# Kernel optimization log

Hardware: AMD Instinct MI355X
Metric: run time of the kernel (lower is better)

## Reference

```python
import jax, jax.numpy as jnp
import numpy as np

EMBED_DIM = 1024
VOCAB = 32000
B, S = 4, 4096


def setup_inputs() -> dict:
    key = jax.random.key(0)
    ks = jax.random.split(key, 6)
    scale = 1.0 / np.sqrt(EMBED_DIM)
    x = jax.random.randint(ks[0], (B, S), 0, VOCAB, dtype=jnp.int64)
    embed = jax.random.normal(ks[1], (VOCAB, EMBED_DIM), dtype=jnp.float32)
    qkv_w = jax.random.normal(ks[2], (EMBED_DIM, 3 * EMBED_DIM), dtype=jnp.float32) * scale
    qkv_b = jnp.zeros((3 * EMBED_DIM,), dtype=jnp.float32)
    out_w = jax.random.normal(ks[3], (EMBED_DIM, VOCAB), dtype=jnp.float32) * scale
    out_b = jnp.zeros((VOCAB,), dtype=jnp.float32)
    return {"x": x, "embed": embed, "qkv_w": qkv_w, "qkv_b": qkv_b,
            "out_w": out_w, "out_b": out_b}


def reference(x, embed, qkv_w, qkv_b, out_w, out_b):
    h = embed[x]                                   # [B,S,D] token embedding lookup
    qkv = h @ qkv_w + qkv_b                        # [B,S,3D]
    qkv = qkv.reshape(B, S, 3, EMBED_DIM)
    q, k, v = qkv[:, :, 0], qkv[:, :, 1], qkv[:, :, 2]
    logits = jnp.einsum('bqd,bkd->bqk', q, k) / jnp.sqrt(jnp.float32(EMBED_DIM))
    attn = jax.nn.softmax(logits, axis=-1)         # [B,S,S] full score matrix (as in source)
    out = jnp.einsum('bqk,bkd->bqd', attn, v)
    h = out + h                                    # residual
    # source applies output projection then slices last token; equivalent to
    # projecting the last-token hidden only.
    return h[:, -1, :] @ out_w + out_b             # [B, vocab]
```

## Files before the change

kernel.cpp:

```cpp
#include <hip/hip_runtime.h>
#include <hip/hip_bf16.h>

typedef __bf16 bf16;
typedef __bf16 bf16x4 __attribute__((ext_vector_type(4)));
typedef __bf16 bf16x8 __attribute__((ext_vector_type(8)));
typedef float floatx4 __attribute__((ext_vector_type(4)));

#define EMBED 1024
#define VOCAB 32000
#define BB    4
#define SS    4096
#define NTOK  (BB * SS)
#define NKV   2048
#define NSEG  16

__device__ __forceinline__ void async_copy16(void* lds, const void* g) {
    __builtin_amdgcn_global_load_lds(
        (const __attribute__((address_space(1))) unsigned int*)g,
        (__attribute__((address_space(3))) unsigned int*)lds, 16, 0, 0);
}

__global__ void gather_embed(const int* __restrict__ x,
                             const float* __restrict__ embed,
                             bf16* __restrict__ h,
                             float* __restrict__ h_last,
                             float* __restrict__ h_final) {
    int t = blockIdx.x;
    int tid = threadIdx.x;
    int row = x[t];
    const float4* src = (const float4*)(embed + (size_t)row * EMBED);
    float4 v = src[tid];
    bf16x4 o; o.x = (bf16)v.x; o.y = (bf16)v.y; o.z = (bf16)v.z; o.w = (bf16)v.w;
    *(bf16x4*)(h + (size_t)t * EMBED + tid * 4) = o;
    if ((t & (SS - 1)) == SS - 1) {
        int b = t >> 12;
        *(float4*)(h_last  + b * EMBED + tid * 4) = v;
        *(float4*)(h_final + b * EMBED + tid * 4) = v;
    }
}

__global__ void wkvt_transpose(const float* __restrict__ qkv_w,
                               bf16* __restrict__ WkvT) {
    __shared__ float T[32][33];
    int n0 = blockIdx.x * 32, d0 = blockIdx.y * 32;
    int tid = threadIdx.x;
    int c = tid & 31, r = tid >> 5;
#pragma unroll
    for (int i = 0; i < 4; ++i) {
        int d = r + i * 8;
        T[c][d] = qkv_w[(size_t)(d0 + d) * (3 * EMBED) + EMBED + n0 + c];
    }
    __syncthreads();
#pragma unroll
    for (int i = 0; i < 4; ++i) {
        int n = r + i * 8;
        WkvT[(size_t)(n0 + n) * EMBED + d0 + c] = (bf16)T[n][c];
    }
}

__global__ void q_gemm(const float* __restrict__ h_last,
                       const float* __restrict__ qkv_w,
                       float* __restrict__ qpart) {
    __shared__ float hs[BB * 64];
    int tid = threadIdx.x;
    int seg = blockIdx.x, d0 = seg * 64;
    hs[tid] = h_last[(tid >> 6) * EMBED + d0 + (tid & 63)];
    __syncthreads();
    int j0 = tid * 4;
    floatx4 acc[BB];
#pragma unroll
    for (int b = 0; b < BB; ++b) acc[b] = (floatx4)0.0f;
#pragma unroll 4
    for (int dd = 0; dd < 64; ++dd) {
        float4 w = *(const float4*)(qkv_w + (size_t)(d0 + dd) * (3 * EMBED) + j0);
#pragma unroll
        for (int b = 0; b < BB; ++b) {
            float hv = hs[b * 64 + dd];
            acc[b][0] += hv * w.x; acc[b][1] += hv * w.y;
            acc[b][2] += hv * w.z; acc[b][3] += hv * w.w;
        }
    }
#pragma unroll
    for (int b = 0; b < BB; ++b)
        *(floatx4*)(qpart + ((size_t)seg * BB + b) * EMBED + j0) = acc[b];
}

__global__ void q_reduce(const float* __restrict__ qpart,
                         const float* __restrict__ qkv_b,
                         float* __restrict__ q) {
    int k = blockIdx.x * 256 + threadIdx.x;
    int b = k >> 10, d = k & (EMBED - 1);
    float s = qkv_b[d];
#pragma unroll
    for (int sg = 0; sg < NSEG; ++sg) s += qpart[((size_t)sg * BB + b) * EMBED + d];
    q[k] = s;
}

__global__ __launch_bounds__(512, 1) void gemm_kv(
    const bf16* __restrict__ A,
    const bf16* __restrict__ BT,
    const float* __restrict__ bias,
    bf16* __restrict__ C) {
    __shared__ __align__(16) bf16 SA[2][2][256 * 32];
    __shared__ __align__(16) bf16 SB[2][2][256 * 32];

    const int tid  = threadIdx.x;
    const int wave = tid >> 6, lane = tid & 63;
    const int wm = wave >> 2, wn = wave & 3;
    const int l16 = lane & 15, quad = lane >> 4;
    const int swz_l = (l16 & 3) ^ ((l16 >> 2) & 3);
    const int a_base = (wm * 128 + l16) * 32 + (quad ^ swz_l) * 8;
    const int b_base = (wn * 64  + l16) * 32 + (quad ^ swz_l) * 8;

    const bf16* Abase = A  + (size_t)blockIdx.x * 256 * EMBED;
    const bf16* Bbase = BT + (size_t)blockIdx.y * 256 * EMBED;

    floatx4 acc[8][4];
#pragma unroll
    for (int m = 0; m < 8; ++m)
#pragma unroll
        for (int n = 0; n < 4; ++n) acc[m][n] = (floatx4)0.0f;

    bf16x8 af[4], af2[4], bfr[4];

#define STG(KH, KT) do { \
    int c_ = wave * 128 + lane; \
    int r_ = c_ >> 2, sw_ = (r_ & 3) ^ ((r_ >> 2) & 3); \
    size_t go_ = (size_t)r_ * EMBED + (KT) * 64 + (KH) * 32 + ((c_ & 3) ^ sw_) * 8; \
    async_copy16(&SA[KH][(KT) & 1][c_ * 8], Abase + go_); \
    async_copy16(&SB[KH][(KT) & 1][c_ * 8], Bbase + go_); \
    c_ += 64; r_ = c_ >> 2; sw_ = (r_ & 3) ^ ((r_ >> 2) & 3); \
    go_ = (size_t)r_ * EMBED + (KT) * 64 + (KH) * 32 + ((c_ & 3) ^ sw_) * 8; \
    async_copy16(&SA[KH][(KT) & 1][c_ * 8], Abase + go_); \
    async_copy16(&SB[KH][(KT) & 1][c_ * 8], Bbase + go_); \
} while (0)

#define NOSTG() do { } while (0)

#define HSTEP(KH, PAR, STG_BODY, WN) do { \
    __builtin_amdgcn_sched_barrier(0); \
    asm volatile("s_waitcnt vmcnt(" #WN ")" ::: "memory"); \
    __builtin_amdgcn_s_barrier(); \
    __builtin_amdgcn_sched_barrier(0); \
    STG_BODY; \
    { const bf16* pa_ = &SA[KH][PAR][a_base]; \
      const bf16* pb_ = &SB[KH][PAR][b_base]; \
      _Pragma("unroll") \
      for (int i_ = 0; i_ < 4; ++i_) af [i_] = *(const bf16x8*)(pa_ + i_ * 512); \
      _Pragma("unroll") \
      for (int i_ = 0; i_ < 4; ++i_) bfr[i_] = *(const bf16x8*)(pb_ + i_ * 512); \
      _Pragma("unroll") \
      for (int i_ = 0; i_ < 4; ++i_) af2[i_] = *(const bf16x8*)(pa_ + 2048 + i_ * 512); } \
    __builtin_amdgcn_s_setprio(1); \
    _Pragma("unroll") \
    for (int mf_ = 0; mf_ < 4; ++mf_) \
    _Pragma("unroll") \
    for (int nf_ = 0; nf_ < 4; ++nf_) \
        acc[mf_][nf_] = __builtin_amdgcn_mfma_f32_16x16x32_bf16( \
            af[mf_], bfr[nf_], acc[mf_][nf_], 0, 0, 0); \
    _Pragma("unroll") \
    for (int mf_ = 0; mf_ < 4; ++mf_) \
    _Pragma("unroll") \
    for (int nf_ = 0; nf_ < 4; ++nf_) \
        acc[4 + mf_][nf_] = __builtin_amdgcn_mfma_f32_16x16x32_bf16( \
            af2[mf_], bfr[nf_], acc[4 + mf_][nf_], 0, 0, 0); \
    __builtin_amdgcn_s_setprio(0); \
} while (0)

    STG(0, 0); STG(1, 0); STG(0, 1);

#pragma unroll 1
    for (int kk = 0; kk < 7; ++kk) {
        const int t1 = 2 * kk + 1;
        HSTEP(0, 0, STG(1, t1),     8);
        HSTEP(1, 0, STG(0, t1 + 1), 8);
        HSTEP(0, 1, STG(1, t1 + 1), 8);
        HSTEP(1, 1, STG(0, t1 + 2), 8);
    }
    HSTEP(0, 0, STG(1, 15), 8);
    HSTEP(1, 0, NOSTG(),    8);
    HSTEP(0, 1, NOSTG(),    4);
    HSTEP(1, 1, NOSTG(),    0);

    const int crow0 = blockIdx.x * 256 + wm * 128;
    const int ccol0 = blockIdx.y * 256 + wn * 64;
    float bsv[4];
#pragma unroll
    for (int nf = 0; nf < 4; ++nf) bsv[nf] = bias[ccol0 + nf * 16 + l16];
#pragma unroll
    for (int fm = 0; fm < 8; ++fm)
#pragma unroll
        for (int nf = 0; nf < 4; ++nf) {
            int col = ccol0 + nf * 16 + l16;
#pragma unroll
            for (int r = 0; r < 4; ++r) {
                int row = crow0 + fm * 16 + quad * 4 + r;
                C[(size_t)row * NKV + col] = (bf16)(acc[fm][nf][r] + bsv[nf]);
            }
        }
#undef STG
#undef NOSTG
#undef HSTEP
}

__global__ void attn_logits(const bf16* __restrict__ KV,
                            const float* __restrict__ q,
                            float* __restrict__ logits) {
    __shared__ float qs[EMBED];
    int b = blockIdx.x >> 10;
    int t = (blockIdx.x & 1023) * 4 + (threadIdx.x >> 6);
    int lane = threadIdx.x & 63;
    *(float4*)(qs + threadIdx.x * 4) = *(const float4*)(q + b * EMBED + threadIdx.x * 4);
    __syncthreads();
    const bf16* Krow = KV + (size_t)(b * SS + t) * NKV;
    float sum = 0.0f;
#pragma unroll
    for (int i = 0; i < 2; ++i) {
        int d0 = i * 512 + lane * 8;
        bf16x8 kv8 = *(const bf16x8*)(Krow + d0);
        float4 qa = *(const float4*)(qs + d0);
        float4 qc = *(const float4*)(qs + d0 + 4);
        sum += qa.x * (float)kv8[0] + qa.y * (float)kv8[1] +
               qa.z * (float)kv8[2] + qa.w * (float)kv8[3] +
               qc.x * (float)kv8[4] + qc.y * (float)kv8[5] +
               qc.z * (float)kv8[6] + qc.w * (float)kv8[7];
    }
#pragma unroll
    for (int o = 32; o; o >>= 1) sum += __shfl_down(sum, o);
    if (lane == 0) logits[b * SS + t] = sum * 0.03125f;
}

__global__ void softmax_k(const float* __restrict__ logits,
                          float* __restrict__ wts) {
    int b = blockIdx.x, tid = threadIdx.x;
    __shared__ float redm[16], reds[16];
    const float* l = logits + b * SS;
    float x0 = l[tid], x1 = l[tid + 1024], x2 = l[tid + 2048], x3 = l[tid + 3072];
    float m = fmaxf(fmaxf(x0, x1), fmaxf(x2, x3));
#pragma unroll
    for (int o = 32; o; o >>= 1) m = fmaxf(m, __shfl_down(m, o));
    if ((tid & 63) == 0) redm[tid >> 6] = m;
    __syncthreads();
    float M = redm[0];
#pragma unroll
    for (int i = 1; i < 16; ++i) M = fmaxf(M, redm[i]);
    float e0 = expf(x0 - M), e1 = expf(x1 - M), e2 = expf(x2 - M), e3 = expf(x3 - M);
    float s = e0 + e1 + e2 + e3;
#pragma unroll
    for (int o = 32; o; o >>= 1) s += __shfl_down(s, o);
    if ((tid & 63) == 0) reds[tid >> 6] = s;
    __syncthreads();
    float S = 0.0f;
#pragma unroll
    for (int i = 0; i < 16; ++i) S += reds[i];
    float inv = 1.0f / S;
    float* w = wts + b * SS;
    w[tid] = e0 * inv; w[tid + 1024] = e1 * inv;
    w[tid + 2048] = e2 * inv; w[tid + 3072] = e3 * inv;
}

__global__ void attn_av(const bf16* __restrict__ KV,
                        const float* __restrict__ wts,
                        float* __restrict__ avpart) {
    int b = blockIdx.x >> 6, ts = blockIdx.x & 63;
    int tid = threadIdx.x;
    __shared__ float wsh[64];
    if (tid < 64) wsh[tid] = wts[b * SS + ts * 64 + tid];
    __syncthreads();
    int d = tid * 4;
    const bf16* Vb = KV + (size_t)(b * SS + ts * 64) * NKV + EMBED + d;
    float a0 = 0, a1 = 0, a2 = 0, a3 = 0;
#pragma unroll 4
    for (int j = 0; j < 64; ++j) {
        bf16x4 v = *(const bf16x4*)(Vb + (size_t)j * NKV);
        float w = wsh[j];
        a0 += w * (float)v.x; a1 += w * (float)v.y;
        a2 += w * (float)v.z; a3 += w * (float)v.w;
    }
    float4 o; o.x = a0; o.y = a1; o.z = a2; o.w = a3;
    *(float4*)(avpart + (size_t)(b * 64 + ts) * EMBED + d) = o;
}

__global__ void av_reduce(const float* __restrict__ avpart,
                          float* __restrict__ h_final) {
    int i = blockIdx.x * 256 + threadIdx.x;
    int b = i >> 10, d = i & (EMBED - 1);
    float s = 0.0f;
#pragma unroll
    for (int ts = 0; ts < 64; ++ts)
        s += avpart[(size_t)(b * 64 + ts) * EMBED + d];
    h_final[i] += s;
}

__global__ void out_gemm(const float* __restrict__ h_final,
                         const float* __restrict__ out_w,
                         float* __restrict__ opart) {
    __shared__ float hs[BB * 64];
    int tid = threadIdx.x;
    int seg = blockIdx.y, d0 = seg * 64;
    hs[tid] = h_final[(tid >> 6) * EMBED + d0 + (tid & 63)];
    __syncthreads();
    int j0 = blockIdx.x * 1024 + tid * 4;
    if (j0 >= VOCAB) return;
    floatx4 acc[BB];
#pragma unroll
    for (int b = 0; b < BB; ++b) acc[b] = (floatx4)0.0f;
#pragma unroll 4
    for (int dd = 0; dd < 64; ++dd) {
        float4 w = *(const float4*)(out_w + (size_t)(d0 + dd) * VOCAB + j0);
#pragma unroll
        for (int b = 0; b < BB; ++b) {
            float hv = hs[b * 64 + dd];
            acc[b][0] += hv * w.x; acc[b][1] += hv * w.y;
            acc[b][2] += hv * w.z; acc[b][3] += hv * w.w;
        }
    }
#pragma unroll
    for (int b = 0; b < BB; ++b)
        *(floatx4*)(opart + ((size_t)seg * BB + b) * VOCAB + j0) = acc[b];
}

__global__ void out_reduce(const float* __restrict__ opart,
                           const float* __restrict__ out_b,
                           float* __restrict__ out) {
    int i = blockIdx.x * 256 + threadIdx.x;
    if (i >= BB * VOCAB) return;
    int b = i / VOCAB, j = i - b * VOCAB;
    float s = out_b[j];
#pragma unroll
    for (int sg = 0; sg < NSEG; ++sg) s += opart[((size_t)sg * BB + b) * VOCAB + j];
    out[i] = s;
}

extern "C" void kernel_launch(void* const* d_in, const int* in_sizes, int n_in,
                              void* d_out, int out_size, void* d_ws, size_t ws_size,
                              hipStream_t stream) {
    const int*   x      = (const int*)d_in[0];
    const float* embed  = (const float*)d_in[1];
    const float* qkv_w  = (const float*)d_in[2];
    const float* qkv_b  = (const float*)d_in[3];
    const float* out_w  = (const float*)d_in[4];
    const float* out_b  = (const float*)d_in[5];
    float* out = (float*)d_out;

    char* ws = (char*)d_ws;
    bf16*  h       = (bf16*)(ws);
    float* avpart  = (float*)(ws);
    float* opart   = (float*)(ws);
    bf16*  KV      = (bf16*)(ws + 33554432);
    bf16*  WkvT    = (bf16*)(ws + 100663296);
    float* h_last  = (float*)(ws + 104857600);
    float* h_final = (float*)(ws + 104873984);
    float* q       = (float*)(ws + 104890368);
    float* logits  = (float*)(ws + 104906752);
    float* wts     = (float*)(ws + 104972288);
    float* qpart   = (float*)(ws + 105037824);

    gather_embed<<<NTOK, 256, 0, stream>>>(x, embed, h, h_last, h_final);
    wkvt_transpose<<<dim3(64, 32), 256, 0, stream>>>(qkv_w, WkvT);
    q_gemm<<<NSEG, 256, 0, stream>>>(h_last, qkv_w, qpart);
    q_reduce<<<16, 256, 0, stream>>>(qpart, qkv_b, q);
    gemm_kv<<<dim3(NTOK / 256, NKV / 256), 512, 0, stream>>>(
        h, WkvT, qkv_b + EMBED, KV);
    attn_logits<<<SS, 256, 0, stream>>>(KV, q, logits);
    softmax_k<<<BB, 1024, 0, stream>>>(logits, wts);
    attn_av<<<256, 256, 0, stream>>>(KV, wts, avpart);
    av_reduce<<<16, 256, 0, stream>>>(avpart, h_final);
    out_gemm<<<dim3(32, NSEG), 256, 0, stream>>>(h_final, out_w, opart);
    out_reduce<<<(BB * VOCAB + 255) / 256, 256, 0, stream>>>(opart, out_b, out);
}
```

Measured before the change: 404.2 us.

## Deepen KV GEMM pipeline to four LDS stages with register double-buffered fragments

Reworks the K/V projection GEMM main loop so LDS holds four 32-wide K slices in flight instead of two double-buffered halves. Operand fragments for the next slice are read into a second register set while MFMAs run on the current set, so LDS reads overlap matrix math. The cost is more VGPRs for the duplicated fragments and an extra lgkmcnt wait per step. Register pressure could cause spills, and the synchronization has to stay correct.

```diff
diff --git a/kernel.cpp b/kernel.cpp
--- a/kernel.cpp
+++ b/kernel.cpp
@@ -101,8 +101,8 @@
     const bf16* __restrict__ BT,
     const float* __restrict__ bias,
     bf16* __restrict__ C) {
-    __shared__ __align__(16) bf16 SA[2][2][256 * 32];
-    __shared__ __align__(16) bf16 SB[2][2][256 * 32];
+    __shared__ __align__(16) bf16 SA[4][8192];
+    __shared__ __align__(16) bf16 SB[4][8192];
 
     const int tid  = threadIdx.x;
     const int wave = tid >> 6, lane = tid & 63;
@@ -121,66 +121,89 @@
 #pragma unroll
         for (int n = 0; n < 4; ++n) acc[m][n] = (floatx4)0.0f;
 
-    bf16x8 af[4], af2[4], bfr[4];
-
-#define STG(KH, KT) do { \
+    bf16x8 af0[4], af20[4], bf0[4];
+    bf16x8 af1[4], af21[4], bf1[4];
+
+#define STG(H) do { \
     int c_ = wave * 128 + lane; \
     int r_ = c_ >> 2, sw_ = (r_ & 3) ^ ((r_ >> 2) & 3); \
-    size_t go_ = (size_t)r_ * EMBED + (KT) * 64 + (KH) * 32 + ((c_ & 3) ^ sw_) * 8; \
-    async_copy16(&SA[KH][(KT) & 1][c_ * 8], Abase + go_); \
-    async_copy16(&SB[KH][(KT) & 1][c_ * 8], Bbase + go_); \
+    size_t go_ = (size_t)r_ * EMBED + (H) * 32 + ((c_ & 3) ^ sw_) * 8; \
+    async_copy16(&SA[(H) & 3][c_ * 8], Abase + go_); \
+    async_copy16(&SB[(H) & 3][c_ * 8], Bbase + go_); \
     c_ += 64; r_ = c_ >> 2; sw_ = (r_ & 3) ^ ((r_ >> 2) & 3); \
-    go_ = (size_t)r_ * EMBED + (KT) * 64 + (KH) * 32 + ((c_ & 3) ^ sw_) * 8; \
-    async_copy16(&SA[KH][(KT) & 1][c_ * 8], Abase + go_); \
-    async_copy16(&SB[KH][(KT) & 1][c_ * 8], Bbase + go_); \
+    go_ = (size_t)r_ * EMBED + (H) * 32 + ((c_ & 3) ^ sw_) * 8; \
+    async_copy16(&SA[(H) & 3][c_ * 8], Abase + go_); \
+    async_copy16(&SB[(H) & 3][c_ * 8], Bbase + go_); \
 } while (0)
 
-#define NOSTG() do { } while (0)
-
-#define HSTEP(KH, PAR, STG_BODY, WN) do { \
+#define RDF(H, AF, AF2, BF) do { \
+    const bf16* pa_ = &SA[(H) & 3][0] + a_base; \
+    const bf16* pb_ = &SB[(H) & 3][0] + b_base; \
+    _Pragma("unroll") \
+    for (int i_ = 0; i_ < 4; ++i_) AF[i_]  = *(const bf16x8*)(pa_ + i_ * 512); \
+    _Pragma("unroll") \
+    for (int i_ = 0; i_ < 4; ++i_) BF[i_]  = *(const bf16x8*)(pb_ + i_ * 512); \
+    _Pragma("unroll") \
+    for (int i_ = 0; i_ < 4; ++i_) AF2[i_] = *(const bf16x8*)(pa_ + 2048 + i_ * 512); \
+} while (0)
+
+#define MFMAH(AF, AF2, BF) do { \
+    __builtin_amdgcn_s_setprio(1); \
+    _Pragma("unroll") \
+    for (int mf_ = 0; mf_ < 4; ++mf_) \
+    _Pragma("unroll") \
+    for (int nf_ = 0; nf_ < 4; ++nf_) \
+        acc[mf_][nf_] = __builtin_amdgcn_mfma_f32_16x16x32_bf16( \
+            AF[mf_], BF[nf_], acc[mf_][nf_], 0, 0, 0); \
+    _Pragma("unroll") \
+    for (int mf_ = 0; mf_ < 4; ++mf_) \
+    _Pragma("unroll") \
+    for (int nf_ = 0; nf_ < 4; ++nf_) \
+        acc[4 + mf_][nf_] = __builtin_amdgcn_mfma_f32_16x16x32_bf16( \
+            AF2[mf_], BF[nf_], acc[4 + mf_][nf_], 0, 0, 0); \
+    __builtin_amdgcn_s_setprio(0); \
+} while (0)
+
+#define SYNC(VM) do { \
     __builtin_amdgcn_sched_barrier(0); \
-    asm volatile("s_waitcnt vmcnt(" #WN ")" ::: "memory"); \
+    asm volatile("s_waitcnt lgkmcnt(0)" ::: "memory"); \
+    asm volatile("s_waitcnt vmcnt(" #VM ")" ::: "memory"); \
     __builtin_amdgcn_s_barrier(); \
     __builtin_amdgcn_sched_barrier(0); \
-    STG_BODY; \
-    { const bf16* pa_ = &SA[KH][PAR][a_base]; \
-      const bf16* pb_ = &SB[KH][PAR][b_base]; \
-      _Pragma("unroll") \
-      for (int i_ = 0; i_ < 4; ++i_) af [i_] = *(const bf16x8*)(pa_ + i_ * 512); \
-      _Pragma("unroll") \
-      for (int i_ = 0; i_ < 4; ++i_) bfr[i_] = *(const bf16x8*)(pb_ + i_ * 512); \
-      _Pragma("unroll") \
-      for (int i_ = 0; i_ < 4; ++i_) af2[i_] = *(const bf16x8*)(pa_ + 2048 + i_ * 512); } \
-    __builtin_amdgcn_s_setprio(1); \
-    _Pragma("unroll") \
-    for (int mf_ = 0; mf_ < 4; ++mf_) \
-    _Pragma("unroll") \
-    for (int nf_ = 0; nf_ < 4; ++nf_) \
-        acc[mf_][nf_] = __builtin_amdgcn_mfma_f32_16x16x32_bf16( \
-            af[mf_], bfr[nf_], acc[mf_][nf_], 0, 0, 0); \
-    _Pragma("unroll") \
-    for (int mf_ = 0; mf_ < 4; ++mf_) \
-    _Pragma("unroll") \
-    for (int nf_ = 0; nf_ < 4; ++nf_) \
-        acc[4 + mf_][nf_] = __builtin_amdgcn_mfma_f32_16x16x32_bf16( \
-            af2[mf_], bfr[nf_], acc[4 + mf_][nf_], 0, 0, 0); \
-    __builtin_amdgcn_s_setprio(0); \
 } while (0)
 
-    STG(0, 0); STG(1, 0); STG(0, 1);
+    STG(0); STG(1); STG(2); STG(3);
+    __builtin_amdgcn_sched_barrier(0);
+    asm volatile("s_waitcnt vmcnt(8)" ::: "memory");
+    __builtin_amdgcn_s_barrier();
+    __builtin_amdgcn_sched_barrier(0);
+    RDF(0, af0, af20, bf0);
+    __builtin_amdgcn_sched_barrier(0);
+    asm volatile("s_waitcnt lgkmcnt(0)" ::: "memory");
+    __builtin_amdgcn_s_barrier();
+    __builtin_amdgcn_sched_barrier(0);
 
 #pragma unroll 1
-    for (int kk = 0; kk < 7; ++kk) {
-        const int t1 = 2 * kk + 1;
-        HSTEP(0, 0, STG(1, t1),     8);
-        HSTEP(1, 0, STG(0, t1 + 1), 8);
-        HSTEP(0, 1, STG(1, t1 + 1), 8);
-        HSTEP(1, 1, STG(0, t1 + 2), 8);
-    }
-    HSTEP(0, 0, STG(1, 15), 8);
-    HSTEP(1, 0, NOSTG(),    8);
-    HSTEP(0, 1, NOSTG(),    4);
-    HSTEP(1, 1, NOSTG(),    0);
+    for (int kk = 0; kk < 14; ++kk) {
+        const int H = 2 * kk;
+        STG(H + 4);
+        RDF(H + 1, af1, af21, bf1);
+        MFMAH(af0, af20, bf0);
+        SYNC(8);
+        STG(H + 5);
+        RDF(H + 2, af0, af20, bf0);
+        MFMAH(af1, af21, bf1);
+        SYNC(8);
+    }
+    RDF(29, af1, af21, bf1);
+    MFMAH(af0, af20, bf0);
+    SYNC(4);
+    RDF(30, af0, af20, bf0);
+    MFMAH(af1, af21, bf1);
+    SYNC(0);
+    RDF(31, af1, af21, bf1);
+    MFMAH(af0, af20, bf0);
+    MFMAH(af1, af21, bf1);
 
     const int crow0 = blockIdx.x * 256 + wm * 128;
     const int ccol0 = blockIdx.y * 256 + wn * 64;
@@ -199,8 +222,9 @@
             }
         }
 #undef STG
-#undef NOSTG
-#undef HSTEP
+#undef RDF
+#undef MFMAH
+#undef SYNC
 }
 
 __global__ void attn_logits(const bf16* __restrict__ KV,
```

After: 415.4 us. 2.8% more time.

## Fuse prep kernels, atomically accumulate AV output, single-pass output projection

Applied to the files above, without the earlier changes.

Merges the embedding gather, K/V weight transpose and Q projection into one launch, with the Q path reading last-token embeddings straight from the table. The attention-value kernel now atomically adds its partial sums into the residual buffer instead of writing partials for a separate reduce. The output projection is rewritten so each block covers 64 vocab columns over the full embedding, reducing within the block and adding the bias, which removes the partial buffer and the reduce kernel. This cuts four launches and the partial-buffer traffic, but the atomics make the summation order nondeterministic and the new GEMM loads out_w with scalar rather than vector reads.

```diff
diff --git a/kernel.cpp b/kernel.cpp
--- a/kernel.cpp
+++ b/kernel.cpp
@@ -20,69 +20,66 @@
         (__attribute__((address_space(3))) unsigned int*)lds, 16, 0, 0);
 }
 
-__global__ void gather_embed(const int* __restrict__ x,
-                             const float* __restrict__ embed,
-                             bf16* __restrict__ h,
-                             float* __restrict__ h_last,
-                             float* __restrict__ h_final) {
-    int t = blockIdx.x;
-    int tid = threadIdx.x;
-    int row = x[t];
-    const float4* src = (const float4*)(embed + (size_t)row * EMBED);
-    float4 v = src[tid];
-    bf16x4 o; o.x = (bf16)v.x; o.y = (bf16)v.y; o.z = (bf16)v.z; o.w = (bf16)v.w;
-    *(bf16x4*)(h + (size_t)t * EMBED + tid * 4) = o;
-    if ((t & (SS - 1)) == SS - 1) {
-        int b = t >> 12;
-        *(float4*)(h_last  + b * EMBED + tid * 4) = v;
-        *(float4*)(h_final + b * EMBED + tid * 4) = v;
-    }
-}
-
-__global__ void wkvt_transpose(const float* __restrict__ qkv_w,
-                               bf16* __restrict__ WkvT) {
+__global__ void prep(const int* __restrict__ x,
+                     const float* __restrict__ embed,
+                     const float* __restrict__ qkv_w,
+                     bf16* __restrict__ h,
+                     float* __restrict__ h_final,
+                     bf16* __restrict__ WkvT,
+                     float* __restrict__ qpart) {
     __shared__ float T[32][33];
-    int n0 = blockIdx.x * 32, d0 = blockIdx.y * 32;
-    int tid = threadIdx.x;
-    int c = tid & 31, r = tid >> 5;
-#pragma unroll
-    for (int i = 0; i < 4; ++i) {
-        int d = r + i * 8;
-        T[c][d] = qkv_w[(size_t)(d0 + d) * (3 * EMBED) + EMBED + n0 + c];
-    }
-    __syncthreads();
-#pragma unroll
-    for (int i = 0; i < 4; ++i) {
-        int n = r + i * 8;
-        WkvT[(size_t)(n0 + n) * EMBED + d0 + c] = (bf16)T[n][c];
-    }
-}
-
-__global__ void q_gemm(const float* __restrict__ h_last,
-                       const float* __restrict__ qkv_w,
-                       float* __restrict__ qpart) {
     __shared__ float hs[BB * 64];
-    int tid = threadIdx.x;
-    int seg = blockIdx.x, d0 = seg * 64;
-    hs[tid] = h_last[(tid >> 6) * EMBED + d0 + (tid & 63)];
-    __syncthreads();
-    int j0 = tid * 4;
-    floatx4 acc[BB];
-#pragma unroll
-    for (int b = 0; b < BB; ++b) acc[b] = (floatx4)0.0f;
+    const int blk = blockIdx.x, tid = threadIdx.x;
+
+    if (blk < NTOK) {
+        int row = x[blk];
+        const float4* src = (const float4*)(embed + (size_t)row * EMBED);
+        float4 v = src[tid];
+        bf16x4 o; o.x = (bf16)v.x; o.y = (bf16)v.y; o.z = (bf16)v.z; o.w = (bf16)v.w;
+        *(bf16x4*)(h + (size_t)blk * EMBED + tid * 4) = o;
+        if ((blk & (SS - 1)) == SS - 1) {
+            int b = blk >> 12;
+            *(float4*)(h_final + b * EMBED + tid * 4) = v;
+        }
+    } else if (blk < NTOK + 2048) {
+        int idx = blk - NTOK;
+        int n0 = (idx & 63) * 32, d0 = (idx >> 6) * 32;
+        int c = tid & 31, r = tid >> 5;
+#pragma unroll
+        for (int i = 0; i < 4; ++i) {
+            int d = r + i * 8;
+            T[c][d] = qkv_w[(size_t)(d0 + d) * (3 * EMBED) + EMBED + n0 + c];
+        }
+        __syncthreads();
+#pragma unroll
+        for (int i = 0; i < 4; ++i) {
+            int n = r + i * 8;
+            WkvT[(size_t)(n0 + n) * EMBED + d0 + c] = (bf16)T[n][c];
+        }
+    } else {
+        int seg = blk - (NTOK + 2048), d0 = seg * 64;
+        int b = tid >> 6;
+        int lrow = x[((b + 1) << 12) - 1];
+        hs[tid] = embed[(size_t)lrow * EMBED + d0 + (tid & 63)];
+        __syncthreads();
+        int j0 = tid * 4;
+        floatx4 acc[BB];
+#pragma unroll
+        for (int bb = 0; bb < BB; ++bb) acc[bb] = (floatx4)0.0f;
 #pragma unroll 4
-    for (int dd = 0; dd < 64; ++dd) {
-        float4 w = *(const float4*)(qkv_w + (size_t)(d0 + dd) * (3 * EMBED) + j0);
-#pragma unroll
-        for (int b = 0; b < BB; ++b) {
-            float hv = hs[b * 64 + dd];
-            acc[b][0] += hv * w.x; acc[b][1] += hv * w.y;
-            acc[b][2] += hv * w.z; acc[b][3] += hv * w.w;
-        }
-    }
-#pragma unroll
-    for (int b = 0; b < BB; ++b)
-        *(floatx4*)(qpart + ((size_t)seg * BB + b) * EMBED + j0) = acc[b];
+        for (int dd = 0; dd < 64; ++dd) {
+            float4 w = *(const float4*)(qkv_w + (size_t)(d0 + dd) * (3 * EMBED) + j0);
+#pragma unroll
+            for (int bb = 0; bb < BB; ++bb) {
+                float hv = hs[bb * 64 + dd];
+                acc[bb][0] += hv * w.x; acc[bb][1] += hv * w.y;
+                acc[bb][2] += hv * w.z; acc[bb][3] += hv * w.w;
+            }
+        }
+#pragma unroll
+        for (int bb = 0; bb < BB; ++bb)
+            *(floatx4*)(qpart + ((size_t)seg * BB + bb) * EMBED + j0) = acc[bb];
+    }
 }
 
 __global__ void q_reduce(const float* __restrict__ qpart,
@@ -261,7 +258,7 @@
 
 __global__ void attn_av(const bf16* __restrict__ KV,
                         const float* __restrict__ wts,
-                        float* __restrict__ avpart) {
+                        float* __restrict__ h_final) {
     int b = blockIdx.x >> 6, ts = blockIdx.x & 63;
     int tid = threadIdx.x;
     __shared__ float wsh[64];
@@ -277,59 +274,42 @@
         a0 += w * (float)v.x; a1 += w * (float)v.y;
         a2 += w * (float)v.z; a3 += w * (float)v.w;
     }
-    float4 o; o.x = a0; o.y = a1; o.z = a2; o.w = a3;
-    *(float4*)(avpart + (size_t)(b * 64 + ts) * EMBED + d) = o;
-}
-
-__global__ void av_reduce(const float* __restrict__ avpart,
-                          float* __restrict__ h_final) {
-    int i = blockIdx.x * 256 + threadIdx.x;
-    int b = i >> 10, d = i & (EMBED - 1);
-    float s = 0.0f;
-#pragma unroll
-    for (int ts = 0; ts < 64; ++ts)
-        s += avpart[(size_t)(b * 64 + ts) * EMBED + d];
-    h_final[i] += s;
-}
-
-__global__ void out_gemm(const float* __restrict__ h_final,
-                         const float* __restrict__ out_w,
-                         float* __restrict__ opart) {
-    __shared__ float hs[BB * 64];
+    atomicAdd(h_final + b * EMBED + d + 0, a0);
+    atomicAdd(h_final + b * EMBED + d + 1, a1);
+    atomicAdd(h_final + b * EMBED + d + 2, a2);
+    atomicAdd(h_final + b * EMBED + d + 3, a3);
+}
+
+__global__ void out_gemm2(const float* __restrict__ h_final,
+                          const float* __restrict__ out_w,
+                          const float* __restrict__ out_b,
+                          float* __restrict__ out) {
+    __shared__ float hs[BB * EMBED];
+    __shared__ float red[4][BB][64];
     int tid = threadIdx.x;
-    int seg = blockIdx.y, d0 = seg * 64;
-    hs[tid] = h_final[(tid >> 6) * EMBED + d0 + (tid & 63)];
-    __syncthreads();
-    int j0 = blockIdx.x * 1024 + tid * 4;
-    if (j0 >= VOCAB) return;
-    floatx4 acc[BB];
-#pragma unroll
-    for (int b = 0; b < BB; ++b) acc[b] = (floatx4)0.0f;
+    int j0 = blockIdx.x * 64;
+#pragma unroll
+    for (int i = 0; i < BB * EMBED; i += 256) hs[i + tid] = h_final[i + tid];
+    __syncthreads();
+    int col = tid & 63, r = tid >> 6;
+    int j = j0 + col;
+    float a0 = 0, a1 = 0, a2 = 0, a3 = 0;
 #pragma unroll 4
-    for (int dd = 0; dd < 64; ++dd) {
-        float4 w = *(const float4*)(out_w + (size_t)(d0 + dd) * VOCAB + j0);
-#pragma unroll
-        for (int b = 0; b < BB; ++b) {
-            float hv = hs[b * 64 + dd];
-            acc[b][0] += hv * w.x; acc[b][1] += hv * w.y;
-            acc[b][2] += hv * w.z; acc[b][3] += hv * w.w;
-        }
-    }
-#pragma unroll
-    for (int b = 0; b < BB; ++b)
-        *(floatx4*)(opart + ((size_t)seg * BB + b) * VOCAB + j0) = acc[b];
-}
-
-__global__ void out_reduce(const float* __restrict__ opart,
-                           const float* __restrict__ out_b,
-                           float* __restrict__ out) {
-    int i = blockIdx.x * 256 + threadIdx.x;
-    if (i >= BB * VOCAB) return;
-    int b = i / VOCAB, j = i - b * VOCAB;
-    float s = out_b[j];
-#pragma unroll
-    for (int sg = 0; sg < NSEG; ++sg) s += opart[((size_t)sg * BB + b) * VOCAB + j];
-    out[i] = s;
+    for (int i = 0; i < 256; ++i) {
+        int d = r + i * 4;
+        float w = out_w[(size_t)d * VOCAB + j];
+        a0 += hs[d] * w;
+        a1 += hs[EMBED + d] * w;
+        a2 += hs[2 * EMBED + d] * w;
+        a3 += hs[3 * EMBED + d] * w;
+    }
+    red[r][0][col] = a0; red[r][1][col] = a1;
+    red[r][2][col] = a2; red[r][3][col] = a3;
+    __syncthreads();
+    int b = tid >> 6;
+    float s = out_b[j0 + col] +
+              red[0][b][col] + red[1][b][col] + red[2][b][col] + red[3][b][col];
+    out[b * VOCAB + j0 + col] = s;
 }
 
 extern "C" void kernel_launch(void* const* d_in, const int* in_sizes, int n_in,
@@ -345,27 +325,20 @@
 
     char* ws = (char*)d_ws;
     bf16*  h       = (bf16*)(ws);
-    float* avpart  = (float*)(ws);
-    float* opart   = (float*)(ws);
     bf16*  KV      = (bf16*)(ws + 33554432);
     bf16*  WkvT    = (bf16*)(ws + 100663296);
-    float* h_last  = (float*)(ws + 104857600);
     float* h_final = (float*)(ws + 104873984);
     float* q       = (float*)(ws + 104890368);
     float* logits  = (float*)(ws + 104906752);
     float* wts     = (float*)(ws + 104972288);
     float* qpart   = (float*)(ws + 105037824);
 
-    gather_embed<<<NTOK, 256, 0, stream>>>(x, embed, h, h_last, h_final);
-    wkvt_transpose<<<dim3(64, 32), 256, 0, stream>>>(qkv_w, WkvT);
-    q_gemm<<<NSEG, 256, 0, stream>>>(h_last, qkv_w, qpart);
+    prep<<<NTOK + 2048 + NSEG, 256, 0, stream>>>(x, embed, qkv_w, h, h_final, WkvT, qpart);
     q_reduce<<<16, 256, 0, stream>>>(qpart, qkv_b, q);
     gemm_kv<<<dim3(NTOK / 256, NKV / 256), 512, 0, stream>>>(
         h, WkvT, qkv_b + EMBED, KV);
     attn_logits<<<SS, 256, 0, stream>>>(KV, q, logits);
     softmax_k<<<BB, 1024, 0, stream>>>(logits, wts);
-    attn_av<<<256, 256, 0, stream>>>(KV, wts, avpart);
-    av_reduce<<<16, 256, 0, stream>>>(avpart, h_final);
-    out_gemm<<<dim3(32, NSEG), 256, 0, stream>>>(h_final, out_w, opart);
-    out_reduce<<<(BB * VOCAB + 255) / 256, 256, 0, stream>>>(opart, out_b, out);
-}
+    attn_av<<<256, 256, 0, stream>>>(KV, wts, h_final);
+    out_gemm2<<<VOCAB / 64, 256, 0, stream>>>(h_final, out_w, out_b, out);
+}
```

Result: faster. 390.6 us (-3.4%).
